# Kernel optimization log

Hardware: AMD Instinct MI355X
Metric: run time of the kernel (lower is better)

Reference implementation:

```python
import jax, jax.numpy as jnp
import numpy as np

LEVELS = np.array([8, 5, 5, 5], dtype=np.int64)
BASIS = np.cumprod(np.concatenate([[1], LEVELS[:-1]])).astype(np.int64)  # [1,8,40,200]
N_E = int(np.prod(LEVELS))  # 1000
BN_EPS = 1e-5
BOUND_EPS = 1e-3


def setup_inputs() -> dict:
    key = jax.random.key(0)
    ks = jax.random.split(key, 3)
    B, C, T, E = 32, 512, 4096, 4
    return {
        "z": jax.random.normal(ks[0], (B, C, T), dtype=jnp.float32),
        "W_in": jax.random.normal(ks[1], (C, E), dtype=jnp.float32) * 0.05,
        "b_in": jnp.zeros((E,), dtype=jnp.float32),
        "gamma": jnp.ones((E,), dtype=jnp.float32),
        "beta": jnp.zeros((E,), dtype=jnp.float32),
        "W_out": jax.random.normal(ks[2], (E, C), dtype=jnp.float32) * 0.05,
        "b_out": jnp.zeros((C,), dtype=jnp.float32),
    }


def _round_ste(x):
    return x + jax.lax.stop_gradient(jnp.round(x) - x)


def reference(z, W_in, b_in, gamma, beta, W_out, b_out):
    levels = jnp.asarray(LEVELS, dtype=jnp.float32)      # [E]
    basis = jnp.asarray(BASIS, dtype=jnp.float32)        # [E]
    half_w = jnp.floor(levels / 2.0)                     # levels // 2
    B, C, T = z.shape
    N = B * T

    # preprocess: 'n c t -> (n t) c'
    x = jnp.transpose(z, (0, 2, 1)).reshape(N, C)        # [N, C]
    # project_in
    h = x @ W_in + b_in                                   # [N, E]
    # BatchNorm1d, training mode (biased batch stats)
    mu = jnp.mean(h, axis=0)
    var = jnp.var(h, axis=0)
    h = (h - mu) * jax.lax.rsqrt(var + BN_EPS) * gamma + beta

    # bound + round_ste quantize
    half_l = (levels - 1.0) * (1.0 - BOUND_EPS) / 2.0
    offset = jnp.where(jnp.mod(levels, 2.0) == 0.0, 0.5, 0.0)
    shift = jnp.tan(offset / half_l)
    bounded = jnp.tanh(h + shift) * half_l - offset
    zhat_n = _round_ste(bounded) / half_w                 # [N, E], normalized codes

    # codes -> indices
    idx = jnp.sum((zhat_n * half_w + half_w) * basis, axis=-1).astype(jnp.int32)  # [N]

    # project_out, '(b t) c -> b c t'
    out = zhat_n @ W_out + b_out                          # [N, C]
    zhat = jnp.transpose(out.reshape(B, T, C), (0, 2, 1))  # [B, C, T]

    commit_loss = jnp.mean((z - jax.lax.stop_gradient(zhat)) ** 2)

    # perplexity via counts (avoids [N, n_e] one-hot)
    counts = jnp.zeros((N_E,), dtype=jnp.float32).at[idx].add(1.0)
    e_mean = counts / N
    perplexity = jnp.exp(-jnp.sum(e_mean * jnp.log(e_mean + 1e-10)))

    return zhat, commit_loss, perplexity
```

## Files before the change

### kernel.cpp

```cpp
#include <hip/hip_runtime.h>
#include <math.h>


namespace {
constexpr int Cv = 512, Tv = 4096, Bv = 32;
constexpr int Nv = Bv * Tv;
constexpr long long TOTv = (long long)Nv * Cv;
constexpr int NBA = 2048;
constexpr int NBC = 2048;
constexpr int NCP = 512;

constexpr size_t OFF_H  = 0;
constexpr size_t OFF_G  = OFF_H  + (size_t)Nv * 16;
constexpr size_t OFF_BS = OFF_G  + (size_t)Nv * 16;
constexpr size_t OFF_CN = OFF_BS + (size_t)NBA * 10 * 8;
constexpr size_t OFF_CP = OFF_CN + 32 * 8;
constexpr size_t OFF_CT = OFF_CP + (size_t)NCP * 8;
}

__global__ __launch_bounds__(256, 4) void fsq_kA(
    const float* __restrict__ z, const float* __restrict__ W_in,
    const float* __restrict__ b_in, const float* __restrict__ W_out,
    const float* __restrict__ b_out,
    float* __restrict__ h_ws, float* __restrict__ g_ws, double* __restrict__ bs)
{
    __shared__ float s_wi[512][4];
    __shared__ float s_wo[512][4];
    __shared__ float s_bo[512];
    __shared__ float red[4][8][64];
    __shared__ float redz[2][256];

    const int tid = threadIdx.x;
    const int bid = blockIdx.x;
    const int b = bid >> 6;
    const int t0 = (bid & 63) << 6;
    const int tq = tid & 63;
    const int cs = tid >> 6;
    const int cbase = cs << 7;

    for (int i = tid; i < 512; i += 256) {
        *(float4*)&s_wi[i][0] = *(const float4*)(W_in + i * 4);
        s_wo[i][0] = W_out[i];
        s_wo[i][1] = W_out[512 + i];
        s_wo[i][2] = W_out[1024 + i];
        s_wo[i][3] = W_out[1536 + i];
        s_bo[i] = b_out[i];
    }
    __syncthreads();

    float h0 = 0.f, h1 = 0.f, h2 = 0.f, h3 = 0.f;
    float g0 = 0.f, g1 = 0.f, g2 = 0.f, g3 = 0.f;
    float z2 = 0.f, zb = 0.f;
    const float* zp = z + ((size_t)b * Cv + cbase) * Tv + t0 + tq;
#pragma unroll 8
    for (int i = 0; i < 128; ++i) {
        const float zv = zp[(size_t)i * Tv];
        const float4 wi = *(const float4*)&s_wi[cbase + i][0];
        const float4 wo = *(const float4*)&s_wo[cbase + i][0];
        h0 = fmaf(zv, wi.x, h0); h1 = fmaf(zv, wi.y, h1);
        h2 = fmaf(zv, wi.z, h2); h3 = fmaf(zv, wi.w, h3);
        g0 = fmaf(zv, wo.x, g0); g1 = fmaf(zv, wo.y, g1);
        g2 = fmaf(zv, wo.z, g2); g3 = fmaf(zv, wo.w, g3);
        z2 = fmaf(zv, zv, z2);
        zb = fmaf(zv, s_bo[cbase + i], zb);
    }

    red[cs][0][tq] = h0; red[cs][1][tq] = h1; red[cs][2][tq] = h2; red[cs][3][tq] = h3;
    red[cs][4][tq] = g0; red[cs][5][tq] = g1; red[cs][6][tq] = g2; red[cs][7][tq] = g3;
    redz[0][tid] = z2; redz[1][tid] = zb;
    __syncthreads();
    for (int s = 128; s > 0; s >>= 1) {
        if (tid < s) { redz[0][tid] += redz[0][tid + s]; redz[1][tid] += redz[1][tid + s]; }
        __syncthreads();
    }

    if (tid < 64) {
        float hh[4], gg[4];
#pragma unroll
        for (int k = 0; k < 4; ++k)
            hh[k] = (red[0][k][tid] + red[1][k][tid]) + (red[2][k][tid] + red[3][k][tid]);
#pragma unroll
        for (int k = 0; k < 4; ++k)
            gg[k] = (red[0][4 + k][tid] + red[1][4 + k][tid]) + (red[2][4 + k][tid] + red[3][4 + k][tid]);
        hh[0] += b_in[0]; hh[1] += b_in[1]; hh[2] += b_in[2]; hh[3] += b_in[3];

        const int n = (b << 12) + t0 + tid;
        *(float4*)(h_ws + (size_t)n * 4) = make_float4(hh[0], hh[1], hh[2], hh[3]);
        *(float4*)(g_ws + (size_t)n * 4) = make_float4(gg[0], gg[1], gg[2], gg[3]);

        double st[8];
#pragma unroll
        for (int e = 0; e < 4; ++e) {
            st[e] = (double)hh[e];
            st[4 + e] = (double)hh[e] * (double)hh[e];
        }
#pragma unroll
        for (int k = 0; k < 8; ++k) {
#pragma unroll
            for (int m = 1; m < 64; m <<= 1) st[k] += __shfl_xor(st[k], m, 64);
        }
        if (tid == 0) {
            double* bp = bs + (size_t)bid * 10;
#pragma unroll
            for (int k = 0; k < 8; ++k) bp[k] = st[k];
            bp[8] = (double)redz[0][0];
            bp[9] = (double)redz[1][0];
        }
    }
}

__global__ __launch_bounds__(256) void fsq_kS(
    const float* __restrict__ gamma, const float* __restrict__ beta,
    const float* __restrict__ W_out, const float* __restrict__ b_out,
    const double* __restrict__ bs, double* __restrict__ consts,
    unsigned* __restrict__ counts)
{
    __shared__ double sbuf[15][256];
    const int tid = threadIdx.x;

    for (int i = tid; i < 1000; i += 256) counts[i] = 0;

    double a[10] = {};
    for (int r = tid; r < NBA; r += 256) {
        const double* p = bs + (size_t)r * 10;
#pragma unroll
        for (int k = 0; k < 10; ++k) a[k] += p[k];
    }
#pragma unroll
    for (int k = 0; k < 10; ++k) sbuf[k][tid] = a[k];
    __syncthreads();
    for (int s = 128; s > 0; s >>= 1) {
        if (tid < s) {
#pragma unroll
            for (int k = 0; k < 10; ++k) sbuf[k][tid] += sbuf[k][tid + s];
        }
        __syncthreads();
    }
    double tot[10];
    if (tid == 0) {
#pragma unroll
        for (int k = 0; k < 10; ++k) tot[k] = sbuf[k][0];
    }
    __syncthreads();

    double gr[15] = {};
    for (int c = tid; c < 512; c += 256) {
        const double w0 = (double)W_out[c], w1 = (double)W_out[512 + c];
        const double w2 = (double)W_out[1024 + c], w3 = (double)W_out[1536 + c];
        const double bb = (double)b_out[c];
        gr[0] += w0 * w0; gr[1] += w0 * w1; gr[2] += w0 * w2; gr[3] += w0 * w3;
        gr[4] += w1 * w1; gr[5] += w1 * w2; gr[6] += w1 * w3;
        gr[7] += w2 * w2; gr[8] += w2 * w3; gr[9] += w3 * w3;
        gr[10] += w0 * bb; gr[11] += w1 * bb; gr[12] += w2 * bb; gr[13] += w3 * bb;
        gr[14] += bb * bb;
    }
#pragma unroll
    for (int k = 0; k < 15; ++k) sbuf[k][tid] = gr[k];
    __syncthreads();
    for (int s = 128; s > 0; s >>= 1) {
        if (tid < s) {
#pragma unroll
            for (int k = 0; k < 15; ++k) sbuf[k][tid] += sbuf[k][tid + s];
        }
        __syncthreads();
    }
    if (tid == 0) {
        const double Ninv = 1.0 / (double)Nv;
#pragma unroll
        for (int e = 0; e < 4; ++e) {
            const double mu = tot[e] * Ninv;
            const double var = tot[4 + e] * Ninv - mu * mu;
            const double sc = (double)gamma[e] / sqrt(var + 1e-5);
            consts[e] = sc;
            consts[4 + e] = (double)beta[e] - mu * sc;
        }
        consts[8] = tot[8];
        consts[9] = tot[9];
#pragma unroll
        for (int k = 0; k < 15; ++k) consts[16 + k] = sbuf[k][0];
        constexpr double hl0 = (8.0 - 1.0) * (1.0 - 1e-3) / 2.0;
        consts[31] = tan(0.5 / hl0);
    }
}

__global__ __launch_bounds__(256, 4) void fsq_kC(
    const float* __restrict__ W_out, const float* __restrict__ b_out,
    const float* __restrict__ h_ws, const float* __restrict__ g_ws,
    const double* __restrict__ consts, unsigned* __restrict__ counts,
    double* __restrict__ cp, float* __restrict__ out)
{
    __shared__ float s_wo[128][4];
    __shared__ float s_bo[128];
    __shared__ double sred[256];

    const int tid = threadIdx.x;
    const int bid = blockIdx.x;
    const int b = bid >> 6;
    const int tt = (bid >> 2) & 15;
    const int ch = bid & 3;
    const int c0 = ch << 7;
    const int t0 = tt << 8;
    const int n = (b << 12) + t0 + tid;

    if (tid < 128) {
        const int c = c0 + tid;
        s_wo[tid][0] = W_out[c];
        s_wo[tid][1] = W_out[512 + c];
        s_wo[tid][2] = W_out[1024 + c];
        s_wo[tid][3] = W_out[1536 + c];
        s_bo[tid] = b_out[c];
    }
    __syncthreads();

    const double sc0 = consts[0], sc1 = consts[1], sc2 = consts[2], sc3 = consts[3];
    const double bi0 = consts[4], bi1 = consts[5], bi2 = consts[6], bi3 = consts[7];
    const double shift0 = consts[31];
    constexpr double hl0 = (8.0 - 1.0) * (1.0 - 1e-3) / 2.0;
    constexpr double hl1 = (5.0 - 1.0) * (1.0 - 1e-3) / 2.0;

    const float4 hv = *(const float4*)(h_ws + (size_t)n * 4);
    const double hn0 = fma((double)hv.x, sc0, bi0);
    const double hn1 = fma((double)hv.y, sc1, bi1);
    const double hn2 = fma((double)hv.z, sc2, bi2);
    const double hn3 = fma((double)hv.w, sc3, bi3);
    const double r0 = rint(tanh(hn0 + shift0) * hl0 - 0.5);
    const double r1 = rint(tanh(hn1) * hl1);
    const double r2 = rint(tanh(hn2) * hl1);
    const double r3 = rint(tanh(hn3) * hl1);
    const double zd0 = r0 * 0.25, zd1 = r1 * 0.5, zd2 = r2 * 0.5, zd3 = r3 * 0.5;
    const float zn0 = (float)zd0, zn1 = (float)zd1, zn2 = (float)zd2, zn3 = (float)zd3;

    if (ch == 0) {
        const int code = ((int)r0 + 4) + ((int)r1 + 2) * 8 + ((int)r2 + 2) * 40
                       + ((int)r3 + 2) * 200;
        atomicAdd(&counts[code], 1u);
        const float4 gv = *(const float4*)(g_ws + (size_t)n * 4);
        const double cg = zd0 * (double)gv.x + zd1 * (double)gv.y
                        + zd2 * (double)gv.z + zd3 * (double)gv.w;
        double q = consts[16 + 14]
                 + 2.0 * (zd0 * consts[16 + 10] + zd1 * consts[16 + 11]
                        + zd2 * consts[16 + 12] + zd3 * consts[16 + 13])
                 + zd0 * zd0 * consts[16 + 0] + zd1 * zd1 * consts[16 + 4]
                 + zd2 * zd2 * consts[16 + 7] + zd3 * zd3 * consts[16 + 9]
                 + 2.0 * (zd0 * zd1 * consts[16 + 1] + zd0 * zd2 * consts[16 + 2]
                        + zd0 * zd3 * consts[16 + 3] + zd1 * zd2 * consts[16 + 5]
                        + zd1 * zd3 * consts[16 + 6] + zd2 * zd3 * consts[16 + 8]);
        sred[tid] = q - 2.0 * cg;
        __syncthreads();
        for (int s = 128; s > 0; s >>= 1) {
            if (tid < s) sred[tid] += sred[tid + s];
            __syncthreads();
        }
        if (tid == 0) cp[(b << 4) + tt] = sred[0];
    }

    float* op = out + ((size_t)b * Cv + c0) * Tv + t0 + tid;
#pragma unroll 8
    for (int i = 0; i < 128; ++i) {
        const float4 wo = *(const float4*)&s_wo[i][0];
        float v = fmaf(zn0, wo.x, fmaf(zn1, wo.y, fmaf(zn2, wo.z, fmaf(zn3, wo.w, s_bo[i]))));
        op[(size_t)i * Tv] = v;
    }
}

__global__ __launch_bounds__(256) void fsq_kD(
    const double* __restrict__ cp, const double* __restrict__ consts,
    const unsigned* __restrict__ counts, float* __restrict__ out, int out_size)
{
    __shared__ double r1[256], r2[256];
    const int tid = threadIdx.x;
    double c_ = cp[tid] + cp[tid + 256];
    double pl = 0.0;
    for (int i = tid; i < 1000; i += 256) {
        const double em = (double)counts[i] / (double)Nv;
        pl += em * log(em + 1e-10);
    }
    r1[tid] = c_; r2[tid] = pl;
    __syncthreads();
    for (int s = 128; s > 0; s >>= 1) {
        if (tid < s) { r1[tid] += r1[tid + s]; r2[tid] += r2[tid + s]; }
        __syncthreads();
    }
    if (tid == 0) {
        const double commit = (consts[8] - 2.0 * consts[9] + r1[0]) / (double)TOTv;
        out[out_size - 2] = (float)commit;
        out[out_size - 1] = (float)exp(-r2[0]);
    }
}

extern "C" void kernel_launch(void* const* d_in, const int* in_sizes, int n_in,
                              void* d_out, int out_size, void* d_ws, size_t ws_size,
                              hipStream_t stream) {
    const float* z     = (const float*)d_in[0];
    const float* W_in  = (const float*)d_in[1];
    const float* b_in  = (const float*)d_in[2];
    const float* gamma = (const float*)d_in[3];
    const float* beta  = (const float*)d_in[4];
    const float* W_out = (const float*)d_in[5];
    const float* b_out = (const float*)d_in[6];
    float* out = (float*)d_out;

    char* ws = (char*)d_ws;
    float*    h_ws   = (float*)(ws + OFF_H);
    float*    g_ws   = (float*)(ws + OFF_G);
    double*   bs     = (double*)(ws + OFF_BS);
    double*   consts = (double*)(ws + OFF_CN);
    double*   cp     = (double*)(ws + OFF_CP);
    unsigned* counts = (unsigned*)(ws + OFF_CT);

    fsq_kA<<<NBA, 256, 0, stream>>>(z, W_in, b_in, W_out, b_out, h_ws, g_ws, bs);
    fsq_kS<<<1, 256, 0, stream>>>(gamma, beta, W_out, b_out, bs, consts, counts);
    fsq_kC<<<NBC, 256, 0, stream>>>(W_out, b_out, h_ws, g_ws, consts, counts, cp, out);
    fsq_kD<<<1, 256, 0, stream>>>(cp, consts, counts, out, out_size);
}
```

Before: 193.4 us.

## Vectorize z loads and output stores with 4 timesteps per thread

Kernel A now has each thread load float4 of z (four consecutive timesteps) and interleave channels across waves, handling 256 timesteps per block, with 4x fewer blocks. Kernel C likewise processes four tokens per thread and writes float4 outputs, replacing the shared-memory tree reduction with wave shuffles. This widens global memory transactions and cuts block count and reduction overhead, at the cost of more registers (launch bounds lowered to 2) and less parallelism.

```diff
diff --git a/kernel.cpp b/kernel.cpp
--- a/kernel.cpp
+++ b/kernel.cpp
@@ -6,9 +6,9 @@
 constexpr int Cv = 512, Tv = 4096, Bv = 32;
 constexpr int Nv = Bv * Tv;
 constexpr long long TOTv = (long long)Nv * Cv;
-constexpr int NBA = 2048;
-constexpr int NBC = 2048;
-constexpr int NCP = 512;
+constexpr int NBA = 512;
+constexpr int NBC = 512;
+constexpr int NCP = 128;
 
 constexpr size_t OFF_H  = 0;
 constexpr size_t OFF_G  = OFF_H  + (size_t)Nv * 16;
@@ -18,7 +18,7 @@
 constexpr size_t OFF_CT = OFF_CP + (size_t)NCP * 8;
 }
 
-__global__ __launch_bounds__(256, 4) void fsq_kA(
+__global__ __launch_bounds__(256, 2) void fsq_kA(
     const float* __restrict__ z, const float* __restrict__ W_in,
     const float* __restrict__ b_in, const float* __restrict__ W_out,
     const float* __restrict__ b_out,
@@ -27,16 +27,16 @@
     __shared__ float s_wi[512][4];
     __shared__ float s_wo[512][4];
     __shared__ float s_bo[512];
-    __shared__ float red[4][8][64];
-    __shared__ float redz[2][256];
+    __shared__ float red_h[4][256][4];
+    __shared__ float red_g[4][256][4];
+    __shared__ double s_st[4][10];
 
     const int tid = threadIdx.x;
+    const int lane = tid & 63;
+    const int w = tid >> 6;
     const int bid = blockIdx.x;
-    const int b = bid >> 6;
-    const int t0 = (bid & 63) << 6;
-    const int tq = tid & 63;
-    const int cs = tid >> 6;
-    const int cbase = cs << 7;
+    const int b = bid >> 4;
+    const int t0 = (bid & 15) << 8;
 
     for (int i = tid; i < 512; i += 256) {
         *(float4*)&s_wi[i][0] = *(const float4*)(W_in + i * 4);
@@ -48,65 +48,82 @@
     }
     __syncthreads();
 
-    float h0 = 0.f, h1 = 0.f, h2 = 0.f, h3 = 0.f;
-    float g0 = 0.f, g1 = 0.f, g2 = 0.f, g3 = 0.f;
+    float h[4][4] = {}, g[4][4] = {};
     float z2 = 0.f, zb = 0.f;
-    const float* zp = z + ((size_t)b * Cv + cbase) * Tv + t0 + tq;
-#pragma unroll 8
-    for (int i = 0; i < 128; ++i) {
-        const float zv = zp[(size_t)i * Tv];
-        const float4 wi = *(const float4*)&s_wi[cbase + i][0];
-        const float4 wo = *(const float4*)&s_wo[cbase + i][0];
-        h0 = fmaf(zv, wi.x, h0); h1 = fmaf(zv, wi.y, h1);
-        h2 = fmaf(zv, wi.z, h2); h3 = fmaf(zv, wi.w, h3);
-        g0 = fmaf(zv, wo.x, g0); g1 = fmaf(zv, wo.y, g1);
-        g2 = fmaf(zv, wo.z, g2); g3 = fmaf(zv, wo.w, g3);
-        z2 = fmaf(zv, zv, z2);
-        zb = fmaf(zv, s_bo[cbase + i], zb);
-    }
-
-    red[cs][0][tq] = h0; red[cs][1][tq] = h1; red[cs][2][tq] = h2; red[cs][3][tq] = h3;
-    red[cs][4][tq] = g0; red[cs][5][tq] = g1; red[cs][6][tq] = g2; red[cs][7][tq] = g3;
-    redz[0][tid] = z2; redz[1][tid] = zb;
-    __syncthreads();
-    for (int s = 128; s > 0; s >>= 1) {
-        if (tid < s) { redz[0][tid] += redz[0][tid + s]; redz[1][tid] += redz[1][tid + s]; }
-        __syncthreads();
-    }
-
-    if (tid < 64) {
-        float hh[4], gg[4];
-#pragma unroll
-        for (int k = 0; k < 4; ++k)
-            hh[k] = (red[0][k][tid] + red[1][k][tid]) + (red[2][k][tid] + red[3][k][tid]);
-#pragma unroll
-        for (int k = 0; k < 4; ++k)
-            gg[k] = (red[0][4 + k][tid] + red[1][4 + k][tid]) + (red[2][4 + k][tid] + red[3][4 + k][tid]);
-        hh[0] += b_in[0]; hh[1] += b_in[1]; hh[2] += b_in[2]; hh[3] += b_in[3];
-
-        const int n = (b << 12) + t0 + tid;
-        *(float4*)(h_ws + (size_t)n * 4) = make_float4(hh[0], hh[1], hh[2], hh[3]);
-        *(float4*)(g_ws + (size_t)n * 4) = make_float4(gg[0], gg[1], gg[2], gg[3]);
-
-        double st[8];
-#pragma unroll
-        for (int e = 0; e < 4; ++e) {
-            st[e] = (double)hh[e];
-            st[4 + e] = (double)hh[e] * (double)hh[e];
-        }
-#pragma unroll
-        for (int k = 0; k < 8; ++k) {
-#pragma unroll
-            for (int m = 1; m < 64; m <<= 1) st[k] += __shfl_xor(st[k], m, 64);
-        }
-        if (tid == 0) {
-            double* bp = bs + (size_t)bid * 10;
-#pragma unroll
-            for (int k = 0; k < 8; ++k) bp[k] = st[k];
-            bp[8] = (double)redz[0][0];
-            bp[9] = (double)redz[1][0];
-        }
-    }
+    const float* zp = z + (size_t)b * Cv * Tv + t0 + lane * 4;
+#pragma unroll 4
+    for (int ci = 0; ci < 128; ++ci) {
+        const int c = ci * 4 + w;
+        const float4 zv = *(const float4*)(zp + (size_t)c * Tv);
+        const float4 wi = *(const float4*)&s_wi[c][0];
+        const float4 wo = *(const float4*)&s_wo[c][0];
+        const float bo = s_bo[c];
+        const float zr[4] = {zv.x, zv.y, zv.z, zv.w};
+#pragma unroll
+        for (int j = 0; j < 4; ++j) {
+            h[j][0] = fmaf(zr[j], wi.x, h[j][0]);
+            h[j][1] = fmaf(zr[j], wi.y, h[j][1]);
+            h[j][2] = fmaf(zr[j], wi.z, h[j][2]);
+            h[j][3] = fmaf(zr[j], wi.w, h[j][3]);
+            g[j][0] = fmaf(zr[j], wo.x, g[j][0]);
+            g[j][1] = fmaf(zr[j], wo.y, g[j][1]);
+            g[j][2] = fmaf(zr[j], wo.z, g[j][2]);
+            g[j][3] = fmaf(zr[j], wo.w, g[j][3]);
+            z2 = fmaf(zr[j], zr[j], z2);
+        }
+        zb = fmaf((zr[0] + zr[1]) + (zr[2] + zr[3]), bo, zb);
+    }
+
+#pragma unroll
+    for (int j = 0; j < 4; ++j) {
+        *(float4*)&red_h[w][lane * 4 + j][0] = make_float4(h[j][0], h[j][1], h[j][2], h[j][3]);
+        *(float4*)&red_g[w][lane * 4 + j][0] = make_float4(g[j][0], g[j][1], g[j][2], g[j][3]);
+    }
+    __syncthreads();
+
+    const float4 ra = *(const float4*)&red_h[0][tid][0];
+    const float4 rb = *(const float4*)&red_h[1][tid][0];
+    const float4 rc = *(const float4*)&red_h[2][tid][0];
+    const float4 rd = *(const float4*)&red_h[3][tid][0];
+    float hh[4];
+    hh[0] = (ra.x + rb.x) + (rc.x + rd.x) + b_in[0];
+    hh[1] = (ra.y + rb.y) + (rc.y + rd.y) + b_in[1];
+    hh[2] = (ra.z + rb.z) + (rc.z + rd.z) + b_in[2];
+    hh[3] = (ra.w + rb.w) + (rc.w + rd.w) + b_in[3];
+    const float4 qa = *(const float4*)&red_g[0][tid][0];
+    const float4 qb = *(const float4*)&red_g[1][tid][0];
+    const float4 qc = *(const float4*)&red_g[2][tid][0];
+    const float4 qd = *(const float4*)&red_g[3][tid][0];
+    float gg[4];
+    gg[0] = (qa.x + qb.x) + (qc.x + qd.x);
+    gg[1] = (qa.y + qb.y) + (qc.y + qd.y);
+    gg[2] = (qa.z + qb.z) + (qc.z + qd.z);
+    gg[3] = (qa.w + qb.w) + (qc.w + qd.w);
+
+    const int n = (b << 12) + t0 + tid;
+    *(float4*)(h_ws + (size_t)n * 4) = make_float4(hh[0], hh[1], hh[2], hh[3]);
+    *(float4*)(g_ws + (size_t)n * 4) = make_float4(gg[0], gg[1], gg[2], gg[3]);
+
+    double st[10];
+#pragma unroll
+    for (int e = 0; e < 4; ++e) {
+        st[e] = (double)hh[e];
+        st[4 + e] = (double)hh[e] * (double)hh[e];
+    }
+    st[8] = (double)z2;
+    st[9] = (double)zb;
+#pragma unroll
+    for (int k = 0; k < 10; ++k) {
+#pragma unroll
+        for (int m = 1; m < 64; m <<= 1) st[k] += __shfl_xor(st[k], m, 64);
+    }
+    if (lane == 0) {
+#pragma unroll
+        for (int k = 0; k < 10; ++k) s_st[w][k] = st[k];
+    }
+    __syncthreads();
+    if (tid < 10)
+        bs[(size_t)bid * 10 + tid] = (s_st[0][tid] + s_st[1][tid]) + (s_st[2][tid] + s_st[3][tid]);
 }
 
 __global__ __launch_bounds__(256) void fsq_kS(
@@ -183,7 +200,7 @@
     }
 }
 
-__global__ __launch_bounds__(256, 4) void fsq_kC(
+__global__ __launch_bounds__(256, 2) void fsq_kC(
     const float* __restrict__ W_out, const float* __restrict__ b_out,
     const float* __restrict__ h_ws, const float* __restrict__ g_ws,
     const double* __restrict__ consts, unsigned* __restrict__ counts,
@@ -191,16 +208,18 @@
 {
     __shared__ float s_wo[128][4];
     __shared__ float s_bo[128];
-    __shared__ double sred[256];
+    __shared__ double s_cp[4];
 
     const int tid = threadIdx.x;
+    const int lane = tid & 63;
+    const int w = tid >> 6;
     const int bid = blockIdx.x;
-    const int b = bid >> 6;
-    const int tt = (bid >> 2) & 15;
-    const int ch = bid & 3;
-    const int c0 = ch << 7;
-    const int t0 = tt << 8;
-    const int n = (b << 12) + t0 + tid;
+    const int b = bid >> 4;
+    const int tt = (bid >> 2) & 3;
+    const int cs = bid & 3;
+    const int c0 = cs << 7;
+    const int t0 = tt << 10;
+    const int n0 = (b << 12) + t0;
 
     if (tid < 128) {
         const int c = c0 + tid;
@@ -218,48 +237,64 @@
     constexpr double hl0 = (8.0 - 1.0) * (1.0 - 1e-3) / 2.0;
     constexpr double hl1 = (5.0 - 1.0) * (1.0 - 1e-3) / 2.0;
 
-    const float4 hv = *(const float4*)(h_ws + (size_t)n * 4);
-    const double hn0 = fma((double)hv.x, sc0, bi0);
-    const double hn1 = fma((double)hv.y, sc1, bi1);
-    const double hn2 = fma((double)hv.z, sc2, bi2);
-    const double hn3 = fma((double)hv.w, sc3, bi3);
-    const double r0 = rint(tanh(hn0 + shift0) * hl0 - 0.5);
-    const double r1 = rint(tanh(hn1) * hl1);
-    const double r2 = rint(tanh(hn2) * hl1);
-    const double r3 = rint(tanh(hn3) * hl1);
-    const double zd0 = r0 * 0.25, zd1 = r1 * 0.5, zd2 = r2 * 0.5, zd3 = r3 * 0.5;
-    const float zn0 = (float)zd0, zn1 = (float)zd1, zn2 = (float)zd2, zn3 = (float)zd3;
-
-    if (ch == 0) {
-        const int code = ((int)r0 + 4) + ((int)r1 + 2) * 8 + ((int)r2 + 2) * 40
-                       + ((int)r3 + 2) * 200;
-        atomicAdd(&counts[code], 1u);
-        const float4 gv = *(const float4*)(g_ws + (size_t)n * 4);
-        const double cg = zd0 * (double)gv.x + zd1 * (double)gv.y
-                        + zd2 * (double)gv.z + zd3 * (double)gv.w;
-        double q = consts[16 + 14]
-                 + 2.0 * (zd0 * consts[16 + 10] + zd1 * consts[16 + 11]
-                        + zd2 * consts[16 + 12] + zd3 * consts[16 + 13])
-                 + zd0 * zd0 * consts[16 + 0] + zd1 * zd1 * consts[16 + 4]
-                 + zd2 * zd2 * consts[16 + 7] + zd3 * zd3 * consts[16 + 9]
-                 + 2.0 * (zd0 * zd1 * consts[16 + 1] + zd0 * zd2 * consts[16 + 2]
-                        + zd0 * zd3 * consts[16 + 3] + zd1 * zd2 * consts[16 + 5]
-                        + zd1 * zd3 * consts[16 + 6] + zd2 * zd3 * consts[16 + 8]);
-        sred[tid] = q - 2.0 * cg;
-        __syncthreads();
-        for (int s = 128; s > 0; s >>= 1) {
-            if (tid < s) sred[tid] += sred[tid + s];
-            __syncthreads();
-        }
-        if (tid == 0) cp[(b << 4) + tt] = sred[0];
-    }
-
-    float* op = out + ((size_t)b * Cv + c0) * Tv + t0 + tid;
-#pragma unroll 8
+    float zn[4][4];
+    double qsum = 0.0;
+#pragma unroll
+    for (int j = 0; j < 4; ++j) {
+        const int n = n0 + tid * 4 + j;
+        const float4 hv = *(const float4*)(h_ws + (size_t)n * 4);
+        const double hn0 = fma((double)hv.x, sc0, bi0);
+        const double hn1 = fma((double)hv.y, sc1, bi1);
+        const double hn2 = fma((double)hv.z, sc2, bi2);
+        const double hn3 = fma((double)hv.w, sc3, bi3);
+        const double r0 = rint(tanh(hn0 + shift0) * hl0 - 0.5);
+        const double r1 = rint(tanh(hn1) * hl1);
+        const double r2 = rint(tanh(hn2) * hl1);
+        const double r3 = rint(tanh(hn3) * hl1);
+        const double zd0 = r0 * 0.25, zd1 = r1 * 0.5, zd2 = r2 * 0.5, zd3 = r3 * 0.5;
+        zn[j][0] = (float)zd0; zn[j][1] = (float)zd1;
+        zn[j][2] = (float)zd2; zn[j][3] = (float)zd3;
+        if (cs == 0) {
+            const int code = ((int)r0 + 4) + ((int)r1 + 2) * 8 + ((int)r2 + 2) * 40
+                           + ((int)r3 + 2) * 200;
+            atomicAdd(&counts[code], 1u);
+            const float4 gv = *(const float4*)(g_ws + (size_t)n * 4);
+            const double cg = zd0 * (double)gv.x + zd1 * (double)gv.y
+                            + zd2 * (double)gv.z + zd3 * (double)gv.w;
+            double q = consts[16 + 14]
+                     + 2.0 * (zd0 * consts[16 + 10] + zd1 * consts[16 + 11]
+                            + zd2 * consts[16 + 12] + zd3 * consts[16 + 13])
+                     + zd0 * zd0 * consts[16 + 0] + zd1 * zd1 * consts[16 + 4]
+                     + zd2 * zd2 * consts[16 + 7] + zd3 * zd3 * consts[16 + 9]
+                     + 2.0 * (zd0 * zd1 * consts[16 + 1] + zd0 * zd2 * consts[16 + 2]
+                            + zd0 * zd3 * consts[16 + 3] + zd1 * zd2 * consts[16 + 5]
+                            + zd1 * zd3 * consts[16 + 6] + zd2 * zd3 * consts[16 + 8]);
+            qsum += q - 2.0 * cg;
+        }
+    }
+
+#pragma unroll
+    for (int m = 1; m < 64; m <<= 1) qsum += __shfl_xor(qsum, m, 64);
+    if (lane == 0) s_cp[w] = qsum;
+    __syncthreads();
+    if (tid == 0 && cs == 0)
+        cp[b * 4 + tt] = (s_cp[0] + s_cp[1]) + (s_cp[2] + s_cp[3]);
+
+    float* op = out + ((size_t)b * Cv + c0) * Tv + t0 + tid * 4;
+#pragma unroll 4
     for (int i = 0; i < 128; ++i) {
         const float4 wo = *(const float4*)&s_wo[i][0];
-        float v = fmaf(zn0, wo.x, fmaf(zn1, wo.y, fmaf(zn2, wo.z, fmaf(zn3, wo.w, s_bo[i]))));
-        op[(size_t)i * Tv] = v;
+        const float bo = s_bo[i];
+        float4 o;
+        o.x = fmaf(zn[0][0], wo.x, fmaf(zn[0][1], wo.y,
+              fmaf(zn[0][2], wo.z, fmaf(zn[0][3], wo.w, bo))));
+        o.y = fmaf(zn[1][0], wo.x, fmaf(zn[1][1], wo.y,
+              fmaf(zn[1][2], wo.z, fmaf(zn[1][3], wo.w, bo))));
+        o.z = fmaf(zn[2][0], wo.x, fmaf(zn[2][1], wo.y,
+              fmaf(zn[2][2], wo.z, fmaf(zn[2][3], wo.w, bo))));
+        o.w = fmaf(zn[3][0], wo.x, fmaf(zn[3][1], wo.y,
+              fmaf(zn[3][2], wo.z, fmaf(zn[3][3], wo.w, bo))));
+        *(float4*)(op + (size_t)i * Tv) = o;
     }
 }
 
@@ -269,7 +304,7 @@
 {
     __shared__ double r1[256], r2[256];
     const int tid = threadIdx.x;
-    double c_ = cp[tid] + cp[tid + 256];
+    double c_ = (tid < NCP) ? cp[tid] : 0.0;
     double pl = 0.0;
     for (int i = tid; i < 1000; i += 256) {
         const double em = (double)counts[i] / (double)Nv;
```

After: 195.6 us. Within noise of the previous version (+1.1%).
